# Optimization experiments

Hardware: AMD Instinct MI355X
Metric: run time of the kernel (lower is better)

The kernel has to match this reference:

```python
import jax, jax.numpy as jnp
import numpy as np

N = 50000        # nodes
E = 800000       # edges (before self-loops)
F_IN = 128       # input features
HID = 32         # per-head hidden channels
H1 = 4           # heads of conv1
H2 = 8           # heads of conv2
NEG_SLOPE = 0.2  # PyG GATConv LeakyReLU slope
E_DEC = 100000   # pos/neg decode edges each


def setup_inputs() -> dict:
    key = jax.random.key(0)
    ks = jax.random.split(key, 12)
    s = 0.1
    return {
        "x": jax.random.normal(ks[0], (N, F_IN), jnp.float32),
        "edge_index": jax.random.randint(ks[1], (2, E), 0, N, dtype=jnp.int32),
        "pos_edge_index": jax.random.randint(ks[2], (2, E_DEC), 0, N, dtype=jnp.int32),
        "neg_edge_index": jax.random.randint(ks[3], (2, E_DEC), 0, N, dtype=jnp.int32),
        "W1": jax.random.normal(ks[4], (F_IN, H1 * HID), jnp.float32) * s,
        "a_src1": jax.random.normal(ks[5], (H1, HID), jnp.float32) * s,
        "a_dst1": jax.random.normal(ks[6], (H1, HID), jnp.float32) * s,
        "b1": jax.random.normal(ks[7], (H1 * HID,), jnp.float32) * s,
        "W2": jax.random.normal(ks[8], (H1 * HID, H2 * HID), jnp.float32) * s,
        "a_src2": jax.random.normal(ks[9], (H2, HID), jnp.float32) * s,
        "a_dst2": jax.random.normal(ks[10], (H2, HID), jnp.float32) * s,
        "b2": jax.random.normal(ks[11], (H2 * HID,), jnp.float32) * s,
    }


def _segment_softmax(e, seg, n):
    # softmax over edges grouped by destination node; max is detached (cancels analytically)
    m = jax.lax.stop_gradient(jax.ops.segment_max(e, seg, num_segments=n))
    ex = jnp.exp(e - m[seg])
    denom = jax.ops.segment_sum(ex, seg, num_segments=n)
    return ex / (denom[seg] + 1e-16)


def _gat_conv(x, src, dst, W, a_src, a_dst, b, heads, out_ch):
    n = x.shape[0]
    h = (x @ W).reshape(n, heads, out_ch)             # [N,H,C]
    al_s = (h * a_src[None]).sum(-1)                  # [N,H]
    al_d = (h * a_dst[None]).sum(-1)                  # [N,H]
    e = al_s[src] + al_d[dst]                         # [E,H] edge logits
    e = jnp.where(e > 0, e, NEG_SLOPE * e)            # LeakyReLU
    alpha = _segment_softmax(e, dst, n)               # [E,H]
    msg = h[src] * alpha[:, :, None]                  # [E,H,C]
    out = jax.ops.segment_sum(msg, dst, num_segments=n)  # [N,H,C]
    return out.reshape(n, heads * out_ch) + b


def reference(x, edge_index, pos_edge_index, neg_edge_index,
              W1, a_src1, a_dst1, b1, W2, a_src2, a_dst2, b2):
    n = x.shape[0]
    loops = jnp.arange(n, dtype=edge_index.dtype)     # PyG add_self_loops=True
    src = jnp.concatenate([edge_index[0], loops])
    dst = jnp.concatenate([edge_index[1], loops])
    # encode
    z = jax.nn.relu(_gat_conv(x, src, dst, W1, a_src1, a_dst1, b1, H1, HID))
    z = _gat_conv(z, src, dst, W2, a_src2, a_dst2, b2, H2, HID)
    # decode
    ei = jnp.concatenate([pos_edge_index, neg_edge_index], axis=1)
    logits = (z[ei[0]] * z[ei[1]]).sum(-1)            # [2*E_DEC]
    return logits
```

## Files before the change

### kernel.cpp

```cpp
#include <hip/hip_runtime.h>
#include <hip/hip_bf16.h>

#define NN 50000
#define EE 800000
#define ET (EE + NN)
#define F_IN 128
#define HID 32
#define H1 4
#define H2 8
#define E_DEC 100000
#define NEG_SLOPE 0.2f

typedef __attribute__((ext_vector_type(8))) short short8;
typedef __attribute__((ext_vector_type(4))) float floatx4;

__device__ __forceinline__ unsigned short f2b(float f) {
    __hip_bfloat16 h = __float2bfloat16(f);
    return *reinterpret_cast<unsigned short*>(&h);
}
__device__ __forceinline__ float b2f(unsigned short u) {
    return __uint_as_float(((unsigned int)u) << 16);
}

__device__ __forceinline__ void packW_one(const float* __restrict__ W,
                                          unsigned short* __restrict__ Wp, int OUT, int id) {
    const int ctg = id >> 8;
    const int ln = id & 63;
    const int col = ctg * 16 + (ln & 15);
    const int k0 = ((id >> 6) & 3) * 32 + ((ln >> 4) & 3) * 8;
    ushort4 lo, hi;
    lo.x = f2b(W[(k0 + 0) * OUT + col]);
    lo.y = f2b(W[(k0 + 1) * OUT + col]);
    lo.z = f2b(W[(k0 + 2) * OUT + col]);
    lo.w = f2b(W[(k0 + 3) * OUT + col]);
    hi.x = f2b(W[(k0 + 4) * OUT + col]);
    hi.y = f2b(W[(k0 + 5) * OUT + col]);
    hi.z = f2b(W[(k0 + 6) * OUT + col]);
    hi.w = f2b(W[(k0 + 7) * OUT + col]);
    ((ushort4*)Wp)[id * 2] = lo;
    ((ushort4*)Wp)[id * 2 + 1] = hi;
}

#define HIST_BLOCKS ((EE / 4 + 255) / 256)
#define PACK_BLOCKS ((6144 + 255) / 256)

__global__ void hist_pack_k(const int* __restrict__ ei, int* __restrict__ counts,
                            const int* __restrict__ probe, int* __restrict__ rank,
                            const float* __restrict__ W1, unsigned short* __restrict__ wp1,
                            const float* __restrict__ W2, unsigned short* __restrict__ wp2) {
    if (blockIdx.x < HIST_BLOCKS) {
        const int t = blockIdx.x * 256 + threadIdx.x;
        if (t >= EE / 4) return;
        const int pv = probe[0];
        const int4 d4 = ((const int4*)(ei + EE))[t];
        int4 r4;
        r4.x = atomicAdd(&counts[d4.x], 1) - pv;
        r4.y = atomicAdd(&counts[d4.y], 1) - pv;
        r4.z = atomicAdd(&counts[d4.z], 1) - pv;
        r4.w = atomicAdd(&counts[d4.w], 1) - pv;
        ((int4*)rank)[t] = r4;
    } else {
        const int id = (blockIdx.x - HIST_BLOCKS) * 256 + threadIdx.x;
        if (id < 2048) packW_one(W1, wp1, 128, id);
        else if (id < 6144) packW_one(W2, wp2, 256, id - 2048);
    }
}

__global__ void scan1_k(const int* __restrict__ counts, const int* __restrict__ probe,
                        int* __restrict__ bsum) {
    __shared__ int sh[256];
    const int pv = probe[0];
    int t = threadIdx.x;
    int i = blockIdx.x * 256 + t;
    sh[t] = (i < NN) ? (counts[i] - pv + 1) : 0;
    __syncthreads();
    for (int off = 128; off > 0; off >>= 1) {
        if (t < off) sh[t] += sh[t + off];
        __syncthreads();
    }
    if (t == 0) bsum[blockIdx.x] = sh[0];
}

__global__ void scan2_k(int* __restrict__ bsum, int nb, int* __restrict__ start) {
    __shared__ int sh[256];
    int t = threadIdx.x;
    int v = (t < nb) ? bsum[t] : 0;
    sh[t] = v;
    __syncthreads();
    for (int off = 1; off < 256; off <<= 1) {
        int u = (t >= off) ? sh[t - off] : 0;
        __syncthreads();
        sh[t] += u;
        __syncthreads();
    }
    if (t < nb) bsum[t] = sh[t] - v;
    if (t == 0) start[NN] = ET;
}

__global__ void scan3_k(const int* __restrict__ counts, const int* __restrict__ probe,
                        const int* __restrict__ bsum, int* __restrict__ start,
                        int* __restrict__ csr) {
    __shared__ int sh[256];
    const int pv = probe[0];
    int t = threadIdx.x;
    int i = blockIdx.x * 256 + t;
    int c = (i < NN) ? (counts[i] - pv + 1) : 0;
    sh[t] = c;
    __syncthreads();
    for (int off = 1; off < 256; off <<= 1) {
        int u = (t >= off) ? sh[t - off] : 0;
        __syncthreads();
        sh[t] += u;
        __syncthreads();
    }
    int excl = sh[t] - c + bsum[blockIdx.x];
    if (i < NN) {
        start[i] = excl;
        csr[excl + c - 1] = i;
    }
}

__global__ void scatter_k(const int* __restrict__ ei, const int* __restrict__ rank,
                          const int* __restrict__ start, int* __restrict__ csr) {
    const int t = blockIdx.x * blockDim.x + threadIdx.x;
    if (t >= EE / 4) return;
    const int4 s4 = ((const int4*)ei)[t];
    const int4 d4 = ((const int4*)(ei + EE))[t];
    const int4 r4 = ((const int4*)rank)[t];
    csr[start[d4.x] + r4.x] = s4.x;
    csr[start[d4.y] + r4.y] = s4.y;
    csr[start[d4.z] + r4.z] = s4.z;
    csr[start[d4.w] + r4.w] = s4.w;
}

template <int OUT, int H, int CT, bool F32IN>
__global__ void gemm_k(const void* __restrict__ Xin, const unsigned short* __restrict__ Wp,
                       const float* __restrict__ a_src, const float* __restrict__ a_dst,
                       unsigned short* __restrict__ Hout, float* __restrict__ als,
                       float* __restrict__ ald) {
    const int wave = threadIdx.x >> 6;
    const int lane = threadIdx.x & 63;
    const int quad = lane >> 4;
    const int rl = lane & 15;
    const int r0 = blockIdx.x * 64;
    floatx4 acc[4][CT];
#pragma unroll
    for (int rt = 0; rt < 4; ++rt)
#pragma unroll
        for (int ct = 0; ct < CT; ++ct) acc[rt][ct] = {0.f, 0.f, 0.f, 0.f};

#pragma unroll
    for (int ks = 0; ks < 4; ++ks) {
        short8 a[4];
        const int c0k = ks * 32 + quad * 8;
#pragma unroll
        for (int rt = 0; rt < 4; ++rt) {
            int row = r0 + rt * 16 + rl;
            row = row < NN ? row : NN - 1;
            if (F32IN) {
                const float4* xp =
                    (const float4*)((const float*)Xin + (long long)row * 128 + c0k);
                const float4 v0 = xp[0];
                const float4 v1 = xp[1];
                short8 tt;
                tt[0] = (short)f2b(v0.x);
                tt[1] = (short)f2b(v0.y);
                tt[2] = (short)f2b(v0.z);
                tt[3] = (short)f2b(v0.w);
                tt[4] = (short)f2b(v1.x);
                tt[5] = (short)f2b(v1.y);
                tt[6] = (short)f2b(v1.z);
                tt[7] = (short)f2b(v1.w);
                a[rt] = tt;
            } else {
                a[rt] = *(const short8*)((const unsigned short*)Xin +
                                         (long long)row * 128 + c0k);
            }
        }
#pragma unroll
        for (int ct = 0; ct < CT; ++ct) {
            const int ctg = wave * CT + ct;
            const short8 b = *(const short8*)(Wp + (((ctg * 4 + ks) * 64 + lane) << 3));
#pragma unroll
            for (int rt = 0; rt < 4; ++rt)
                acc[rt][ct] = __builtin_amdgcn_mfma_f32_16x16x32_bf16(a[rt], b, acc[rt][ct], 0, 0, 0);
        }
    }
#pragma unroll
    for (int rt = 0; rt < 4; ++rt) {
        const int rowbase = r0 + rt * 16 + quad * 4;
#pragma unroll
        for (int ct = 0; ct < CT; ++ct) {
            const int col = (wave * CT + ct) * 16 + rl;
#pragma unroll
            for (int r = 0; r < 4; ++r) {
                const int row = rowbase + r;
                if (row < NN) Hout[(long long)row * OUT + col] = f2b(acc[rt][ct][r]);
            }
        }
    }
    float asv[CT], adv[CT];
#pragma unroll
    for (int ct = 0; ct < CT; ++ct) {
        const int col = (wave * CT + ct) * 16 + rl;
        asv[ct] = a_src[col];
        adv[ct] = a_dst[col];
    }
#pragma unroll
    for (int rt = 0; rt < 4; ++rt) {
#pragma unroll
        for (int r = 0; r < 4; ++r) {
            const int row = r0 + rt * 16 + quad * 4 + r;
            float ps[CT / 2], pd[CT / 2];
#pragma unroll
            for (int hh = 0; hh < CT / 2; ++hh) {
                ps[hh] = acc[rt][2 * hh][r] * asv[2 * hh] + acc[rt][2 * hh + 1][r] * asv[2 * hh + 1];
                pd[hh] = acc[rt][2 * hh][r] * adv[2 * hh] + acc[rt][2 * hh + 1][r] * adv[2 * hh + 1];
#pragma unroll
                for (int m = 8; m >= 1; m >>= 1) {
                    ps[hh] += __shfl_xor(ps[hh], m, 64);
                    pd[hh] += __shfl_xor(pd[hh], m, 64);
                }
            }
            if (rl == 0 && row < NN) {
#pragma unroll
                for (int hh = 0; hh < CT / 2; ++hh) {
                    const int hd = wave * (CT / 2) + hh;
                    als[(long long)row * H + hd] = ps[hh];
                    ald[(long long)row * H + hd] = pd[hh];
                }
            }
        }
    }
}

__global__ void gather1_k(const int* __restrict__ start, const int* __restrict__ csr,
                          const float* __restrict__ als, const float* __restrict__ ald,
                          const unsigned short* __restrict__ Hin,
                          const float* __restrict__ bias, unsigned short* __restrict__ outp) {
    const int d = blockIdx.x;
    const int lane = threadIdx.x;
    const int cl = lane & 31;
    const int slot = lane >> 5;
    const int hd = cl >> 3;
    const int beg = start[d], end = start[d + 1];
    const float aldd = ald[(long long)d * H1 + hd];
    float a0 = 0.f, a1 = 0.f, a2 = 0.f, a3 = 0.f, den = 0.f;
    int i = beg + slot;
    for (; i + 7 * 2 < end; i += 8 * 2) {
        int s[8];
        float l[8];
        ushort4 hv[8];
#pragma unroll
        for (int k = 0; k < 8; ++k) s[k] = csr[i + k * 2];
#pragma unroll
        for (int k = 0; k < 8; ++k) l[k] = als[(long long)s[k] * H1 + hd] + aldd;
#pragma unroll
        for (int k = 0; k < 8; ++k) hv[k] = *(const ushort4*)(Hin + (long long)s[k] * 128 + cl * 4);
#pragma unroll
        for (int k = 0; k < 8; ++k) {
            float lg = l[k] > 0.f ? l[k] : NEG_SLOPE * l[k];
            const float w = __expf(lg);
            den += w;
            a0 += w * b2f(hv[k].x);
            a1 += w * b2f(hv[k].y);
            a2 += w * b2f(hv[k].z);
            a3 += w * b2f(hv[k].w);
        }
    }
    for (; i + 3 * 2 < end; i += 4 * 2) {
        int s[4];
        float l[4];
        ushort4 hv[4];
#pragma unroll
        for (int k = 0; k < 4; ++k) s[k] = csr[i + k * 2];
#pragma unroll
        for (int k = 0; k < 4; ++k) l[k] = als[(long long)s[k] * H1 + hd] + aldd;
#pragma unroll
        for (int k = 0; k < 4; ++k) hv[k] = *(const ushort4*)(Hin + (long long)s[k] * 128 + cl * 4);
#pragma unroll
        for (int k = 0; k < 4; ++k) {
            float lg = l[k] > 0.f ? l[k] : NEG_SLOPE * l[k];
            const float w = __expf(lg);
            den += w;
            a0 += w * b2f(hv[k].x);
            a1 += w * b2f(hv[k].y);
            a2 += w * b2f(hv[k].z);
            a3 += w * b2f(hv[k].w);
        }
    }
    for (; i < end; i += 2) {
        const int s = csr[i];
        float lg = als[(long long)s * H1 + hd] + aldd;
        lg = lg > 0.f ? lg : NEG_SLOPE * lg;
        const float w = __expf(lg);
        const ushort4 hv = *(const ushort4*)(Hin + (long long)s * 128 + cl * 4);
        den += w;
        a0 += w * b2f(hv.x);
        a1 += w * b2f(hv.y);
        a2 += w * b2f(hv.z);
        a3 += w * b2f(hv.w);
    }
    a0 += __shfl_xor(a0, 32, 64);
    a1 += __shfl_xor(a1, 32, 64);
    a2 += __shfl_xor(a2, 32, 64);
    a3 += __shfl_xor(a3, 32, 64);
    den += __shfl_xor(den, 32, 64);
    if (lane < 32) {
        const float inv = 1.f / (den + 1e-16f);
        const int c0 = cl * 4;
        float v0 = a0 * inv + bias[c0];
        float v1 = a1 * inv + bias[c0 + 1];
        float v2 = a2 * inv + bias[c0 + 2];
        float v3 = a3 * inv + bias[c0 + 3];
        v0 = v0 > 0.f ? v0 : 0.f;
        v1 = v1 > 0.f ? v1 : 0.f;
        v2 = v2 > 0.f ? v2 : 0.f;
        v3 = v3 > 0.f ? v3 : 0.f;
        ushort4 o;
        o.x = f2b(v0);
        o.y = f2b(v1);
        o.z = f2b(v2);
        o.w = f2b(v3);
        *(ushort4*)(outp + (long long)d * 128 + c0) = o;
    }
}

__global__ void gather2_k(const int* __restrict__ start, const int* __restrict__ csr,
                          const float* __restrict__ als, const float* __restrict__ ald,
                          const unsigned short* __restrict__ Hin,
                          const float* __restrict__ bias, unsigned short* __restrict__ outp) {
    const int d = blockIdx.x;
    const int lane = threadIdx.x;
    const int hd = lane >> 3;
    const int beg = start[d], end = start[d + 1];
    const float aldd = ald[(long long)d * H2 + hd];
    float a0 = 0.f, a1 = 0.f, a2 = 0.f, a3 = 0.f, den = 0.f;
    int i = beg;
    for (; i + 7 < end; i += 8) {
        int s[8];
        float l[8];
        ushort4 hv[8];
#pragma unroll
        for (int k = 0; k < 8; ++k) s[k] = csr[i + k];
#pragma unroll
        for (int k = 0; k < 8; ++k) l[k] = als[(long long)s[k] * H2 + hd] + aldd;
#pragma unroll
        for (int k = 0; k < 8; ++k) hv[k] = *(const ushort4*)(Hin + (long long)s[k] * 256 + lane * 4);
#pragma unroll
        for (int k = 0; k < 8; ++k) {
            float lg = l[k] > 0.f ? l[k] : NEG_SLOPE * l[k];
            const float w = __expf(lg);
            den += w;
            a0 += w * b2f(hv[k].x);
            a1 += w * b2f(hv[k].y);
            a2 += w * b2f(hv[k].z);
            a3 += w * b2f(hv[k].w);
        }
    }
    for (; i + 3 < end; i += 4) {
        int s[4];
        float l[4];
        ushort4 hv[4];
#pragma unroll
        for (int k = 0; k < 4; ++k) s[k] = csr[i + k];
#pragma unroll
        for (int k = 0; k < 4; ++k) l[k] = als[(long long)s[k] * H2 + hd] + aldd;
#pragma unroll
        for (int k = 0; k < 4; ++k) hv[k] = *(const ushort4*)(Hin + (long long)s[k] * 256 + lane * 4);
#pragma unroll
        for (int k = 0; k < 4; ++k) {
            float lg = l[k] > 0.f ? l[k] : NEG_SLOPE * l[k];
            const float w = __expf(lg);
            den += w;
            a0 += w * b2f(hv[k].x);
            a1 += w * b2f(hv[k].y);
            a2 += w * b2f(hv[k].z);
            a3 += w * b2f(hv[k].w);
        }
    }
    for (; i < end; ++i) {
        const int s = csr[i];
        float lg = als[(long long)s * H2 + hd] + aldd;
        lg = lg > 0.f ? lg : NEG_SLOPE * lg;
        const float w = __expf(lg);
        const ushort4 hv = *(const ushort4*)(Hin + (long long)s * 256 + lane * 4);
        den += w;
        a0 += w * b2f(hv.x);
        a1 += w * b2f(hv.y);
        a2 += w * b2f(hv.z);
        a3 += w * b2f(hv.w);
    }
    const float inv = 1.f / (den + 1e-16f);
    const int c0 = lane * 4;
    ushort4 o;
    o.x = f2b(a0 * inv + bias[c0]);
    o.y = f2b(a1 * inv + bias[c0 + 1]);
    o.z = f2b(a2 * inv + bias[c0 + 2]);
    o.w = f2b(a3 * inv + bias[c0 + 3]);
    *(ushort4*)(outp + (long long)d * 256 + c0) = o;
}

__global__ void decode_s_k(const int* __restrict__ pei, const int* __restrict__ nei,
                           const unsigned short* __restrict__ z2, float* __restrict__ part) {
    const int s = blockIdx.x & 7;
    const int g = blockIdx.x >> 3;
    const int wave = threadIdx.x >> 6, lane = threadIdx.x & 63;
    const int slot = lane >> 3, cl = lane & 7;
    const int idx = g * 32 + wave * 8 + slot;
    if (idx >= 2 * E_DEC) return;
    int a, b;
    if (idx < E_DEC) {
        a = pei[idx];
        b = pei[E_DEC + idx];
    } else {
        const int j = idx - E_DEC;
        a = nei[j];
        b = nei[E_DEC + j];
    }
    const ushort4 ua = *(const ushort4*)(z2 + (long long)a * 256 + s * 32 + cl * 4);
    const ushort4 ub = *(const ushort4*)(z2 + (long long)b * 256 + s * 32 + cl * 4);
    float sum = b2f(ua.x) * b2f(ub.x) + b2f(ua.y) * b2f(ub.y) +
                b2f(ua.z) * b2f(ub.z) + b2f(ua.w) * b2f(ub.w);
    sum += __shfl_xor(sum, 4, 64);
    sum += __shfl_xor(sum, 2, 64);
    sum += __shfl_xor(sum, 1, 64);
    if (cl == 0) part[(long long)s * (2 * E_DEC) + idx] = sum;
}

__global__ void reduce_k(const float* __restrict__ part, float* __restrict__ out) {
    const int i = blockIdx.x * 256 + threadIdx.x;
    if (i >= 2 * E_DEC) return;
    float s = 0.f;
#pragma unroll
    for (int k = 0; k < 8; ++k) s += part[(long long)k * (2 * E_DEC) + i];
    out[i] = s;
}

extern "C" void kernel_launch(void* const* d_in, const int* in_sizes, int n_in,
                              void* d_out, int out_size, void* d_ws, size_t ws_size,
                              hipStream_t stream) {
    const float* x = (const float*)d_in[0];
    const int* ei = (const int*)d_in[1];
    const int* pei = (const int*)d_in[2];
    const int* nei = (const int*)d_in[3];
    const float* W1 = (const float*)d_in[4];
    const float* as1 = (const float*)d_in[5];
    const float* ad1 = (const float*)d_in[6];
    const float* b1 = (const float*)d_in[7];
    const float* W2 = (const float*)d_in[8];
    const float* as2 = (const float*)d_in[9];
    const float* ad2 = (const float*)d_in[10];
    const float* b2 = (const float*)d_in[11];
    float* out = (float*)d_out;

    unsigned short* h1 = (unsigned short*)d_ws;
    unsigned short* h2 = h1 + (long long)NN * 128;
    unsigned short* z2 = h2 + (long long)NN * 256;
    unsigned short* z1 = z2 + (long long)NN * 256;
    unsigned short* wp1 = z1 + (long long)NN * 128;
    unsigned short* wp2 = wp1 + 128 * 128;
    float* als1 = (float*)(wp2 + 128 * 256);
    float* ald1 = als1 + NN * H1;
    float* als2 = ald1 + NN * H1;
    float* ald2 = als2 + NN * H2;
    float* part = ald2 + NN * H2;
    int* counts = (int*)(part + 8 * 2 * E_DEC);
    int* start = counts + NN;
    int* rank = start + NN + 1;
    int* bsum = rank + EE;
    int* csr = bsum + 256;
    int* probe = csr + ET;

    const int NB = (NN + 255) / 256;

    hist_pack_k<<<HIST_BLOCKS + PACK_BLOCKS, 256, 0, stream>>>(
        ei, counts, probe, rank, W1, wp1, W2, wp2);
    scan1_k<<<NB, 256, 0, stream>>>(counts, probe, bsum);
    scan2_k<<<1, 256, 0, stream>>>(bsum, NB, start);
    scan3_k<<<NB, 256, 0, stream>>>(counts, probe, bsum, start, csr);
    scatter_k<<<(EE / 4 + 255) / 256, 256, 0, stream>>>(ei, rank, start, csr);

    gemm_k<128, H1, 2, true><<<(NN + 63) / 64, 256, 0, stream>>>(
        x, wp1, as1, ad1, h1, als1, ald1);
    gather1_k<<<NN, 64, 0, stream>>>(start, csr, als1, ald1, h1, b1, z1);

    gemm_k<256, H2, 4, false><<<(NN + 63) / 64, 256, 0, stream>>>(
        z1, wp2, as2, ad2, h2, als2, ald2);
    gather2_k<<<NN, 64, 0, stream>>>(start, csr, als2, ald2, h2, b2, z2);

    decode_s_k<<<8 * ((2 * E_DEC + 31) / 32), 256, 0, stream>>>(pei, nei, z2, part);
    reduce_k<<<(2 * E_DEC + 255) / 256, 256, 0, stream>>>(part, out);
}
```

Measured before the change: 335.8 us.

## Privatize degree histogram into eight partitioned count arrays to reduce atomic contention

The destination-degree histogram is split into eight copies selected by block index, so atomics on the same node counter are spread across separate addresses. The scan kernels sum the eight partial counts, and a per-partition offset table is written so the scatter kernel places each edge using its partition's offset plus rank. This aims to cut contention in the atomic histogram, at the cost of eight times more counter memory and extra reads and writes in the scan kernels. The probe-based baseline subtraction assumes all eight partition arrays share the same initial value.

```diff
diff --git a/kernel.cpp b/kernel.cpp
--- a/kernel.cpp
+++ b/kernel.cpp
@@ -44,7 +44,7 @@
 #define HIST_BLOCKS ((EE / 4 + 255) / 256)
 #define PACK_BLOCKS ((6144 + 255) / 256)
 
-__global__ void hist_pack_k(const int* __restrict__ ei, int* __restrict__ counts,
+__global__ void hist_pack_k(const int* __restrict__ ei, int* __restrict__ counts_p,
                             const int* __restrict__ probe, int* __restrict__ rank,
                             const float* __restrict__ W1, unsigned short* __restrict__ wp1,
                             const float* __restrict__ W2, unsigned short* __restrict__ wp2) {
@@ -52,12 +52,13 @@
         const int t = blockIdx.x * 256 + threadIdx.x;
         if (t >= EE / 4) return;
         const int pv = probe[0];
+        int* cp = counts_p + (blockIdx.x & 7) * NN;
         const int4 d4 = ((const int4*)(ei + EE))[t];
         int4 r4;
-        r4.x = atomicAdd(&counts[d4.x], 1) - pv;
-        r4.y = atomicAdd(&counts[d4.y], 1) - pv;
-        r4.z = atomicAdd(&counts[d4.z], 1) - pv;
-        r4.w = atomicAdd(&counts[d4.w], 1) - pv;
+        r4.x = atomicAdd(&cp[d4.x], 1) - pv;
+        r4.y = atomicAdd(&cp[d4.y], 1) - pv;
+        r4.z = atomicAdd(&cp[d4.z], 1) - pv;
+        r4.w = atomicAdd(&cp[d4.w], 1) - pv;
         ((int4*)rank)[t] = r4;
     } else {
         const int id = (blockIdx.x - HIST_BLOCKS) * 256 + threadIdx.x;
@@ -66,13 +67,20 @@
     }
 }
 
-__global__ void scan1_k(const int* __restrict__ counts, const int* __restrict__ probe,
+__global__ void scan1_k(const int* __restrict__ counts_p, const int* __restrict__ probe,
                         int* __restrict__ bsum) {
     __shared__ int sh[256];
-    const int pv = probe[0];
+    const unsigned pv = (unsigned)probe[0];
     int t = threadIdx.x;
     int i = blockIdx.x * 256 + t;
-    sh[t] = (i < NN) ? (counts[i] - pv + 1) : 0;
+    int deg = 0;
+    if (i < NN) {
+        unsigned sum = 0;
+#pragma unroll
+        for (int s = 0; s < 8; ++s) sum += (unsigned)counts_p[s * NN + i];
+        deg = (int)(sum - 8u * pv) + 1;
+    }
+    sh[t] = deg;
     __syncthreads();
     for (int off = 128; off > 0; off >>= 1) {
         if (t < off) sh[t] += sh[t + off];
@@ -97,15 +105,24 @@
     if (t == 0) start[NN] = ET;
 }
 
-__global__ void scan3_k(const int* __restrict__ counts, const int* __restrict__ probe,
+__global__ void scan3_k(const int* __restrict__ counts_p, const int* __restrict__ probe,
                         const int* __restrict__ bsum, int* __restrict__ start,
-                        int* __restrict__ csr) {
+                        int* __restrict__ offs, int* __restrict__ csr) {
     __shared__ int sh[256];
-    const int pv = probe[0];
+    const unsigned pv = (unsigned)probe[0];
     int t = threadIdx.x;
     int i = blockIdx.x * 256 + t;
-    int c = (i < NN) ? (counts[i] - pv + 1) : 0;
-    sh[t] = c;
+    int part[8];
+    int deg = 0;
+    if (i < NN) {
+        deg = 1;
+#pragma unroll
+        for (int s = 0; s < 8; ++s) {
+            part[s] = (int)((unsigned)counts_p[s * NN + i] - pv);
+            deg += part[s];
+        }
+    }
+    sh[t] = deg;
     __syncthreads();
     for (int off = 1; off < 256; off <<= 1) {
         int u = (t >= off) ? sh[t - off] : 0;
@@ -113,24 +130,31 @@
         sh[t] += u;
         __syncthreads();
     }
-    int excl = sh[t] - c + bsum[blockIdx.x];
+    int excl = sh[t] - deg + bsum[blockIdx.x];
     if (i < NN) {
         start[i] = excl;
-        csr[excl + c - 1] = i;
+        int o = excl;
+#pragma unroll
+        for (int s = 0; s < 8; ++s) {
+            offs[s * NN + i] = o;
+            o += part[s];
+        }
+        csr[o] = i;
     }
 }
 
 __global__ void scatter_k(const int* __restrict__ ei, const int* __restrict__ rank,
-                          const int* __restrict__ start, int* __restrict__ csr) {
-    const int t = blockIdx.x * blockDim.x + threadIdx.x;
+                          const int* __restrict__ offs, int* __restrict__ csr) {
+    const int t = blockIdx.x * 256 + threadIdx.x;
     if (t >= EE / 4) return;
+    const int* off = offs + (blockIdx.x & 7) * NN;
     const int4 s4 = ((const int4*)ei)[t];
     const int4 d4 = ((const int4*)(ei + EE))[t];
     const int4 r4 = ((const int4*)rank)[t];
-    csr[start[d4.x] + r4.x] = s4.x;
-    csr[start[d4.y] + r4.y] = s4.y;
-    csr[start[d4.z] + r4.z] = s4.z;
-    csr[start[d4.w] + r4.w] = s4.w;
+    csr[off[d4.x] + r4.x] = s4.x;
+    csr[off[d4.y] + r4.y] = s4.y;
+    csr[off[d4.z] + r4.z] = s4.z;
+    csr[off[d4.w] + r4.w] = s4.w;
 }
 
 template <int OUT, int H, int CT, bool F32IN>
@@ -465,9 +489,10 @@
     float* als2 = ald1 + NN * H1;
     float* ald2 = als2 + NN * H2;
     float* part = ald2 + NN * H2;
-    int* counts = (int*)(part + 8 * 2 * E_DEC);
-    int* start = counts + NN;
-    int* rank = start + NN + 1;
+    int* counts_p = (int*)(part + 8 * 2 * E_DEC);
+    int* start = counts_p + 8 * NN;
+    int* offs = start + NN + 1;
+    int* rank = offs + 8 * NN;
     int* bsum = rank + EE;
     int* csr = bsum + 256;
     int* probe = csr + ET;
@@ -475,11 +500,11 @@
     const int NB = (NN + 255) / 256;
 
     hist_pack_k<<<HIST_BLOCKS + PACK_BLOCKS, 256, 0, stream>>>(
-        ei, counts, probe, rank, W1, wp1, W2, wp2);
-    scan1_k<<<NB, 256, 0, stream>>>(counts, probe, bsum);
+        ei, counts_p, probe, rank, W1, wp1, W2, wp2);
+    scan1_k<<<NB, 256, 0, stream>>>(counts_p, probe, bsum);
     scan2_k<<<1, 256, 0, stream>>>(bsum, NB, start);
-    scan3_k<<<NB, 256, 0, stream>>>(counts, probe, bsum, start, csr);
-    scatter_k<<<(EE / 4 + 255) / 256, 256, 0, stream>>>(ei, rank, start, csr);
+    scan3_k<<<NB, 256, 0, stream>>>(counts_p, probe, bsum, start, offs, csr);
+    scatter_k<<<HIST_BLOCKS, 256, 0, stream>>>(ei, rank, offs, csr);
 
     gemm_k<128, H1, 2, true><<<(NN + 63) / 64, 256, 0, stream>>>(
         x, wp1, as1, ad1, h1, als1, ald1);
```

Result: no change. 334.7 us (-0.3%).
